# Kernel optimization log

Measured on AMD Instinct MI355X. Metric: run time of the kernel, lower is better.

Reference implementation:

```python
import jax, jax.numpy as jnp
import numpy as np

N_NODES = 50000
N_EDGES = 800000


def setup_inputs() -> dict:
    key = jax.random.key(0)
    ks = jax.random.split(key, 8)
    x = jax.random.normal(ks[0], (N_NODES, 256), dtype=jnp.float32)
    edge_index = jax.random.randint(ks[1], (2, N_EDGES), 0, N_NODES, dtype=jnp.int64)
    edge_weight = jax.random.uniform(ks[2], (N_EDGES,), dtype=jnp.float32)
    # Glorot-style weights for the 3 GCNConv layers: 256->128->64->32
    def glorot(k, fan_in, fan_out):
        s = jnp.sqrt(6.0 / (fan_in + fan_out))
        return jax.random.uniform(k, (fan_in, fan_out), dtype=jnp.float32, minval=-s, maxval=s)
    return {
        "x": x,
        "edge_index": edge_index,
        "edge_weight": edge_weight,
        "W1": glorot(ks[3], 256, 128), "b1": jnp.zeros((128,), jnp.float32),
        "W2": glorot(ks[4], 128, 64),  "b2": jnp.zeros((64,), jnp.float32),
        "W3": glorot(ks[5], 64, 32),   "b3": jnp.zeros((32,), jnp.float32),
    }


def _gcn_forward(x, row, col, ew, params):
    """Stacked GCNConv+ReLU (PyG semantics: add self loops, symmetric norm)."""
    n = x.shape[0]
    loop = jnp.arange(n, dtype=row.dtype)
    row_f = jnp.concatenate([row, loop])            # [E+N] sources
    col_f = jnp.concatenate([col, loop])            # [E+N] targets
    ew_f = jnp.concatenate([ew, jnp.ones((n,), ew.dtype)])
    deg = jax.ops.segment_sum(ew_f, col_f, num_segments=n)
    dinv = jnp.where(deg > 0, jax.lax.rsqrt(deg), 0.0)
    norm = dinv[row_f] * ew_f * dinv[col_f]         # [E+N]
    for W, b in params:
        h = x @ W                                   # [N, d_out] linear first (PyG order)
        msg = h[row_f] * norm[:, None]              # [E+N, d_out] gather + scale
        agg = jax.ops.segment_sum(msg, col_f, num_segments=n)  # scatter-add
        x = jax.nn.relu(agg + b)                    # fused bias + ReLU
    return x


def reference(x, edge_index, edge_weight, W1, b1, W2, b2, W3, b3):
    row, col = edge_index[0], edge_index[1]
    params = [(W1, b1), (W2, b2), (W3, b3)]
    return _gcn_forward(x, row, col, edge_weight, params)
```

## Files before the change

### kernel.cpp

```cpp
#include <hip/hip_runtime.h>
#include <hip/hip_fp16.h>


#define D0 256
#define D1 128
#define D2 64
#define D3 32

#define FIX_SCALE 16777216.0f
#define FIX_INV   (1.0f / 16777216.0f)

typedef _Float16 half8 __attribute__((ext_vector_type(8)));
typedef float floatx4 __attribute__((ext_vector_type(4)));

template <typename SRC>
__device__ __forceinline__ half8 loadA(const SRC* __restrict__ p) {
    if constexpr (sizeof(SRC) == 4) {
        float4 f0 = *(const float4*)p;
        float4 f1 = *(const float4*)(p + 4);
        half8 v;
        v[0] = (_Float16)f0.x; v[1] = (_Float16)f0.y;
        v[2] = (_Float16)f0.z; v[3] = (_Float16)f0.w;
        v[4] = (_Float16)f1.x; v[5] = (_Float16)f1.y;
        v[6] = (_Float16)f1.z; v[7] = (_Float16)f1.w;
        return v;
    } else {
        return *(const half8*)p;
    }
}

template <int K, int BN, typename SRC>
__device__ __forceinline__ void gemm_work(const SRC* __restrict__ X,
                                          const float* __restrict__ W,
                                          _Float16* __restrict__ H, int N,
                                          int w, int totalWaves) {
    constexpr int NC = K / 32;
    constexpr int CG = BN / 32;
    const int lane = threadIdx.x & 63;
    const int quad = lane >> 4;
    const int m = lane & 15;
    const int cg = w & (CG - 1);
    const int nslab = N >> 4;
    const int stride = totalWaves / CG;
    int slab = w / CG;
    if (slab >= nslab) return;
    const int n0 = cg * 32;

    half8 b0[NC], b1[NC];
#pragma unroll
    for (int c = 0; c < NC; ++c) {
#pragma unroll
        for (int j = 0; j < 8; ++j) {
            int k = c * 32 + quad * 8 + j;
            b0[c][j] = (_Float16)W[(size_t)k * BN + n0 + m];
            b1[c][j] = (_Float16)W[(size_t)k * BN + n0 + 16 + m];
        }
    }

    half8 a[NC];
#pragma unroll
    for (int c = 0; c < NC; ++c)
        a[c] = loadA(&X[(size_t)(slab * 16 + m) * K + c * 32 + quad * 8]);

    while (true) {
        const int next = slab + stride;
        half8 an[NC];
        if (next < nslab) {
#pragma unroll
            for (int c = 0; c < NC; ++c)
                an[c] = loadA(&X[(size_t)(next * 16 + m) * K + c * 32 + quad * 8]);
        }

        floatx4 acc0 = (floatx4){0.f, 0.f, 0.f, 0.f};
        floatx4 acc1 = (floatx4){0.f, 0.f, 0.f, 0.f};
#pragma unroll
        for (int c = 0; c < NC; ++c) {
            acc0 = __builtin_amdgcn_mfma_f32_16x16x32_f16(a[c], b0[c], acc0, 0, 0, 0);
            acc1 = __builtin_amdgcn_mfma_f32_16x16x32_f16(a[c], b1[c], acc1, 0, 0, 0);
        }

        const int r0 = slab * 16 + quad * 4;
#pragma unroll
        for (int r = 0; r < 4; ++r) {
            H[(size_t)(r0 + r) * BN + n0 + m]      = (_Float16)acc0[r];
            H[(size_t)(r0 + r) * BN + n0 + 16 + m] = (_Float16)acc1[r];
        }

        if (next >= nslab) break;
        slab = next;
#pragma unroll
        for (int c = 0; c < NC; ++c) a[c] = an[c];
    }
}

__global__ __launch_bounds__(256) void hist_gemm1_kernel(
        const float* __restrict__ x, const float* __restrict__ W1,
        _Float16* __restrict__ h1, int N,
        const int* __restrict__ ei, const float* __restrict__ ew,
        unsigned long long* __restrict__ pk, int* __restrict__ rank, int E,
        int gB) {
    const int b = blockIdx.x;
    if (b < gB) {
        gemm_work<D0, D1, float>(x, W1, h1, N, b * 4 + (threadIdx.x >> 6), gB * 4);
    } else {
        int e = (b - gB) * 256 + threadIdx.x;
        if (e < E) {
            int c = ei[E + e];
            unsigned int wfix = (unsigned int)(ew[e] * FIX_SCALE + 0.5f);
            unsigned long long old =
                atomicAdd(&pk[c], (1ULL << 32) | (unsigned long long)wfix);
            rank[e] = (int)(old >> 32);
        }
    }
}

__global__ __launch_bounds__(256) void scan_reduce(const unsigned long long* __restrict__ pk,
                                                   float* __restrict__ dinv,
                                                   int* __restrict__ cnt,
                                                   int* __restrict__ blockSum, int N) {
    __shared__ int s[256];
    const int t = threadIdx.x;
    const int i = blockIdx.x * 256 + t;
    int v = 0;
    if (i < N) {
        unsigned long long p = pk[i];
        float d = (float)(unsigned int)(p & 0xffffffffULL) * FIX_INV + 1.0f;
        dinv[i] = rsqrtf(d);
        v = (int)(p >> 32);
        cnt[i] = v;
    }
    s[t] = v;
    __syncthreads();
#pragma unroll
    for (int off = 128; off > 0; off >>= 1) {
        if (t < off) s[t] += s[t + off];
        __syncthreads();
    }
    if (t == 0) blockSum[blockIdx.x] = s[0];
}

__global__ __launch_bounds__(256) void scan_apply(const int* __restrict__ cnt,
                                                  const int* __restrict__ blockSum,
                                                  int* __restrict__ row_ptr, int N, int B) {
    __shared__ int bs[256];
    __shared__ int s[256];
    const int t = threadIdx.x;
    bs[t] = (t < B) ? blockSum[t] : 0;
    __syncthreads();
#pragma unroll
    for (int off = 1; off < 256; off <<= 1) {
        int u = (t >= off) ? bs[t - off] : 0;
        __syncthreads();
        bs[t] += u;
        __syncthreads();
    }
    const int myOff = (blockIdx.x > 0) ? bs[blockIdx.x - 1] : 0;
    const int i = blockIdx.x * 256 + t;
    const int v = (i < N) ? cnt[i] : 0;
    s[t] = v;
    __syncthreads();
#pragma unroll
    for (int off = 1; off < 256; off <<= 1) {
        int u = (t >= off) ? s[t - off] : 0;
        __syncthreads();
        s[t] += u;
        __syncthreads();
    }
    if (i < N) row_ptr[i] = s[t] - v + myOff;
    if (blockIdx.x == 0 && t == 0) row_ptr[N] = bs[B - 1];
}

__global__ void fill_kernel(const int* __restrict__ ei, const float* __restrict__ ew,
                            const float* __restrict__ dinv,
                            const int* __restrict__ row_ptr, const int* __restrict__ rank,
                            int2* __restrict__ pairs, int E) {
    int e = blockIdx.x * blockDim.x + threadIdx.x;
    if (e < E) {
        int r = ei[e];
        int c = ei[E + e];
        float w = dinv[r] * ew[e] * dinv[c];
        pairs[row_ptr[c] + rank[e]] = make_int2(r, __float_as_int(w));
    }
}

template <int DIN, int DOUT>
__global__ __launch_bounds__(256) void agg_gemm_kernel(
        const _Float16* __restrict__ H, const int* __restrict__ row_ptr,
        const int2* __restrict__ pairs, const float* __restrict__ dinv,
        const float* __restrict__ bias, const float* __restrict__ W,
        _Float16* __restrict__ Hout, int N) {
    constexpr int TPN = DIN / 8;
    constexpr int NPB = 256 / TPN;
    constexpr int NC  = DIN / 32;
    constexpr int S   = NPB / 16;
    constexpr int T   = DOUT / 16;
    static_assert(S * T == 4, "one tile per wave");
    __shared__ _Float16 sA[NPB][DIN + 8];

    const int tid = threadIdx.x;
    const int g = tid / TPN;
    const int sl = tid % TPN;
    const int node0 = blockIdx.x * NPB;
    const int node = node0 + g;
    const bool valid = node < N;

    const int w = tid >> 6;
    const int lane = tid & 63;
    const int q = lane >> 4;
    const int m = lane & 15;
    const int s = w & (S - 1);
    const int t = w / S;
    half8 bf[NC];
#pragma unroll
    for (int c = 0; c < NC; ++c) {
#pragma unroll
        for (int j = 0; j < 8; ++j)
            bf[c][j] = (_Float16)W[(size_t)(c * 32 + q * 8 + j) * DOUT + t * 16 + m];
    }

    float acc[8];
#pragma unroll
    for (int j = 0; j < 8; ++j) acc[j] = 0.0f;

    int beg = 0, end = 0;
    float di = 0.f;
    half8 uself = (half8){0,0,0,0,0,0,0,0};
    float bb[8];
    if (valid) {
        beg = row_ptr[node];
        end = row_ptr[node + 1];
        di = dinv[node];
        uself = *(const half8*)&H[(size_t)node * DIN + sl * 8];
        *(float4*)&bb[0] = *(const float4*)&bias[sl * 8];
        *(float4*)&bb[4] = *(const float4*)&bias[sl * 8 + 4];
    }

    if (end > beg) {
        const int last = end - 1;
        int2 p0 = pairs[beg];
        int2 p1 = pairs[min(beg + 1, last)];
        int2 p2 = pairs[min(beg + 2, last)];
        int2 p3 = pairs[min(beg + 3, last)];
        int2 p4 = pairs[min(beg + 4, last)];
        half8 u0 = *(const half8*)&H[(size_t)p0.x * DIN + sl * 8];
        half8 u1 = *(const half8*)&H[(size_t)p1.x * DIN + sl * 8];
        half8 u2 = *(const half8*)&H[(size_t)p2.x * DIN + sl * 8];
        half8 u3 = *(const half8*)&H[(size_t)p3.x * DIN + sl * 8];
        for (int k = beg; k < end; ++k) {
            int2 p5 = pairs[min(k + 5, last)];
            half8 u4 = *(const half8*)&H[(size_t)p4.x * DIN + sl * 8];
            float wv = __int_as_float(p0.y);
#pragma unroll
            for (int j = 0; j < 8; ++j) acc[j] = fmaf(wv, (float)u0[j], acc[j]);
            p0 = p1; p1 = p2; p2 = p3; p3 = p4; p4 = p5;
            u0 = u1; u1 = u2; u2 = u3; u3 = u4;
        }
    }

    if (valid) {
        float d2 = di * di;
#pragma unroll
        for (int j = 0; j < 8; ++j) acc[j] = fmaf(d2, (float)uself[j], acc[j]);
        half8 o;
#pragma unroll
        for (int j = 0; j < 8; ++j) o[j] = (_Float16)fmaxf(acc[j] + bb[j], 0.f);
        *(half8*)&sA[g][sl * 8] = o;
    }
    __syncthreads();

    half8 a[NC];
#pragma unroll
    for (int c = 0; c < NC; ++c)
        a[c] = *(const half8*)&sA[s * 16 + m][c * 32 + q * 8];
    floatx4 o4 = (floatx4){0.f, 0.f, 0.f, 0.f};
#pragma unroll
    for (int c = 0; c < NC; ++c)
        o4 = __builtin_amdgcn_mfma_f32_16x16x32_f16(a[c], bf[c], o4, 0, 0, 0);
#pragma unroll
    for (int r = 0; r < 4; ++r) {
        const int nr = node0 + s * 16 + q * 4 + r;
        if (nr < N) Hout[(size_t)nr * DOUT + t * 16 + m] = (_Float16)o4[r];
    }
}

template <int D, typename OUT>
__global__ __launch_bounds__(256) void agg_kernel(const _Float16* __restrict__ H,
                                                  const int* __restrict__ row_ptr,
                                                  const int2* __restrict__ pairs,
                                                  const float* __restrict__ dinv,
                                                  const float* __restrict__ bias,
                                                  OUT* __restrict__ out, int N) {
    constexpr int TPN = D / 8;
    constexpr int NPB = 256 / TPN;
    const int tid = threadIdx.x;
    const int g = tid / TPN;
    const int lane = tid % TPN;
    const int node = blockIdx.x * NPB + g;
    if (node >= N) return;

    const int beg = row_ptr[node];
    const int end = row_ptr[node + 1];
    const float di = dinv[node];
    const half8 uself = *(const half8*)&H[(size_t)node * D + lane * 8];
    float b[8];
    *(float4*)&b[0] = *(const float4*)&bias[lane * 8];
    *(float4*)&b[4] = *(const float4*)&bias[lane * 8 + 4];

    float acc[8];
#pragma unroll
    for (int j = 0; j < 8; ++j) acc[j] = 0.0f;

    if (end > beg) {
        const int last = end - 1;
        int2 p0 = pairs[beg];
        int2 p1 = pairs[min(beg + 1, last)];
        int2 p2 = pairs[min(beg + 2, last)];
        int2 p3 = pairs[min(beg + 3, last)];
        int2 p4 = pairs[min(beg + 4, last)];
        half8 u0 = *(const half8*)&H[(size_t)p0.x * D + lane * 8];
        half8 u1 = *(const half8*)&H[(size_t)p1.x * D + lane * 8];
        half8 u2 = *(const half8*)&H[(size_t)p2.x * D + lane * 8];
        half8 u3 = *(const half8*)&H[(size_t)p3.x * D + lane * 8];
        for (int k = beg; k < end; ++k) {
            int2 p5 = pairs[min(k + 5, last)];
            half8 u4 = *(const half8*)&H[(size_t)p4.x * D + lane * 8];
            float w = __int_as_float(p0.y);
#pragma unroll
            for (int j = 0; j < 8; ++j) acc[j] = fmaf(w, (float)u0[j], acc[j]);
            p0 = p1; p1 = p2; p2 = p3; p3 = p4; p4 = p5;
            u0 = u1; u1 = u2; u2 = u3; u3 = u4;
        }
    }
    const float d2 = di * di;
#pragma unroll
    for (int j = 0; j < 8; ++j) acc[j] = fmaf(d2, (float)uself[j], acc[j]);
#pragma unroll
    for (int j = 0; j < 8; ++j) acc[j] = fmaxf(acc[j] + b[j], 0.f);

    if constexpr (sizeof(OUT) == 2) {
        half8 o;
#pragma unroll
        for (int j = 0; j < 8; ++j) o[j] = (_Float16)acc[j];
        *(half8*)&out[(size_t)node * D + lane * 8] = o;
    } else {
        float* dst = (float*)&out[(size_t)node * D + lane * 8];
        *(float4*)&dst[0] = make_float4(acc[0], acc[1], acc[2], acc[3]);
        *(float4*)&dst[4] = make_float4(acc[4], acc[5], acc[6], acc[7]);
    }
}

extern "C" void kernel_launch(void* const* d_in, const int* in_sizes, int n_in,
                              void* d_out, int out_size, void* d_ws, size_t ws_size,
                              hipStream_t stream) {
    const float* x   = (const float*)d_in[0];
    const int* ei    = (const int*)d_in[1];
    const float* ew  = (const float*)d_in[2];
    const float* W1  = (const float*)d_in[3];
    const float* b1  = (const float*)d_in[4];
    const float* W2  = (const float*)d_in[5];
    const float* b2  = (const float*)d_in[6];
    const float* W3  = (const float*)d_in[7];
    const float* b3  = (const float*)d_in[8];
    float* out = (float*)d_out;

    const int N = in_sizes[0] / D0;
    const int E = in_sizes[2];
    (void)n_in; (void)out_size; (void)ws_size;

    char* ws = (char*)d_ws;
    size_t off = 0;
    auto carve = [&](size_t bytes) -> void* {
        void* p = (void*)(ws + off);
        off += (bytes + 255) & ~(size_t)255;
        return p;
    };
    unsigned long long* pk = (unsigned long long*)carve((size_t)N * 8);
    float* dinv    = (float*)carve((size_t)N * 4);
    int*   cnt     = (int*)carve((size_t)N * 4);
    int*   row_ptr = (int*)carve((size_t)(N + 1) * 4);
    int*   rank    = (int*)carve((size_t)E * 4);
    int*   bsum    = (int*)carve(256 * 4);
    int2*  pairs   = (int2*)carve((size_t)E * 8);
    _Float16* bufH = (_Float16*)carve((size_t)N * D1 * 2);
    _Float16* bufO = (_Float16*)carve((size_t)N * D1 * 2);

    _Float16* h1 = bufH;
    _Float16* h2 = bufO;
    _Float16* h3 = bufH;

    const int eb = (E + 255) / 256;
    const int scanB = (N + 255) / 256;
    const int gB = 768;

    hipMemsetAsync(pk, 0, (size_t)N * 8, stream);
    hist_gemm1_kernel<<<gB + eb, 256, 0, stream>>>(
        x, W1, h1, N, ei, ew, pk, rank, E, gB);

    scan_reduce<<<scanB, 256, 0, stream>>>(pk, dinv, cnt, bsum, N);
    scan_apply<<<scanB, 256, 0, stream>>>(cnt, bsum, row_ptr, N, scanB);
    fill_kernel<<<eb, 256, 0, stream>>>(ei, ew, dinv, row_ptr, rank, pairs, E);

    agg_gemm_kernel<D1, D2><<<(N + 15) / 16, 256, 0, stream>>>(
        h1, row_ptr, pairs, dinv, b1, W2, h2, N);

    agg_gemm_kernel<D2, D3><<<(N + 31) / 32, 256, 0, stream>>>(
        h2, row_ptr, pairs, dinv, b2, W3, h3, N);

    agg_kernel<D3, float><<<(N + 63) / 64, 256, 0, stream>>>(
        h3, row_ptr, pairs, dinv, b3, out, N);
}
```

Baseline: 263.0 us.

## Move layer-1 GEMM into fill kernel with LDS double-buffered X staging

The first-layer GEMM is moved out of the histogram kernel and co-launched with the CSR fill kernel, so the atomic histogram runs alone and the GEMM overlaps the scatter fill instead. The GEMM is also rewritten so a whole block stages a 16-row slab of X into shared memory as fp16, with double buffering, and its four waves each compute a different 32-column group. This aims to get coalesced X loads and to balance the mixed kernels better, at the cost of block-wide syncs and more LDS use.

Result: faster. 253.9 us (-3.5%).

```diff
diff --git a/kernel.cpp b/kernel.cpp
--- a/kernel.cpp
+++ b/kernel.cpp
@@ -13,104 +13,16 @@
 typedef _Float16 half8 __attribute__((ext_vector_type(8)));
 typedef float floatx4 __attribute__((ext_vector_type(4)));
 
-template <typename SRC>
-__device__ __forceinline__ half8 loadA(const SRC* __restrict__ p) {
-    if constexpr (sizeof(SRC) == 4) {
-        float4 f0 = *(const float4*)p;
-        float4 f1 = *(const float4*)(p + 4);
-        half8 v;
-        v[0] = (_Float16)f0.x; v[1] = (_Float16)f0.y;
-        v[2] = (_Float16)f0.z; v[3] = (_Float16)f0.w;
-        v[4] = (_Float16)f1.x; v[5] = (_Float16)f1.y;
-        v[6] = (_Float16)f1.z; v[7] = (_Float16)f1.w;
-        return v;
-    } else {
-        return *(const half8*)p;
-    }
-}
-
-template <int K, int BN, typename SRC>
-__device__ __forceinline__ void gemm_work(const SRC* __restrict__ X,
-                                          const float* __restrict__ W,
-                                          _Float16* __restrict__ H, int N,
-                                          int w, int totalWaves) {
-    constexpr int NC = K / 32;
-    constexpr int CG = BN / 32;
-    const int lane = threadIdx.x & 63;
-    const int quad = lane >> 4;
-    const int m = lane & 15;
-    const int cg = w & (CG - 1);
-    const int nslab = N >> 4;
-    const int stride = totalWaves / CG;
-    int slab = w / CG;
-    if (slab >= nslab) return;
-    const int n0 = cg * 32;
-
-    half8 b0[NC], b1[NC];
-#pragma unroll
-    for (int c = 0; c < NC; ++c) {
-#pragma unroll
-        for (int j = 0; j < 8; ++j) {
-            int k = c * 32 + quad * 8 + j;
-            b0[c][j] = (_Float16)W[(size_t)k * BN + n0 + m];
-            b1[c][j] = (_Float16)W[(size_t)k * BN + n0 + 16 + m];
-        }
-    }
-
-    half8 a[NC];
-#pragma unroll
-    for (int c = 0; c < NC; ++c)
-        a[c] = loadA(&X[(size_t)(slab * 16 + m) * K + c * 32 + quad * 8]);
-
-    while (true) {
-        const int next = slab + stride;
-        half8 an[NC];
-        if (next < nslab) {
-#pragma unroll
-            for (int c = 0; c < NC; ++c)
-                an[c] = loadA(&X[(size_t)(next * 16 + m) * K + c * 32 + quad * 8]);
-        }
-
-        floatx4 acc0 = (floatx4){0.f, 0.f, 0.f, 0.f};
-        floatx4 acc1 = (floatx4){0.f, 0.f, 0.f, 0.f};
-#pragma unroll
-        for (int c = 0; c < NC; ++c) {
-            acc0 = __builtin_amdgcn_mfma_f32_16x16x32_f16(a[c], b0[c], acc0, 0, 0, 0);
-            acc1 = __builtin_amdgcn_mfma_f32_16x16x32_f16(a[c], b1[c], acc1, 0, 0, 0);
-        }
-
-        const int r0 = slab * 16 + quad * 4;
-#pragma unroll
-        for (int r = 0; r < 4; ++r) {
-            H[(size_t)(r0 + r) * BN + n0 + m]      = (_Float16)acc0[r];
-            H[(size_t)(r0 + r) * BN + n0 + 16 + m] = (_Float16)acc1[r];
-        }
-
-        if (next >= nslab) break;
-        slab = next;
-#pragma unroll
-        for (int c = 0; c < NC; ++c) a[c] = an[c];
-    }
-}
-
-__global__ __launch_bounds__(256) void hist_gemm1_kernel(
-        const float* __restrict__ x, const float* __restrict__ W1,
-        _Float16* __restrict__ h1, int N,
+__global__ __launch_bounds__(256) void hist_kernel(
         const int* __restrict__ ei, const float* __restrict__ ew,
-        unsigned long long* __restrict__ pk, int* __restrict__ rank, int E,
-        int gB) {
-    const int b = blockIdx.x;
-    if (b < gB) {
-        gemm_work<D0, D1, float>(x, W1, h1, N, b * 4 + (threadIdx.x >> 6), gB * 4);
-    } else {
-        int e = (b - gB) * 256 + threadIdx.x;
-        if (e < E) {
-            int c = ei[E + e];
-            unsigned int wfix = (unsigned int)(ew[e] * FIX_SCALE + 0.5f);
-            unsigned long long old =
-                atomicAdd(&pk[c], (1ULL << 32) | (unsigned long long)wfix);
-            rank[e] = (int)(old >> 32);
-        }
+        unsigned long long* __restrict__ pk, int* __restrict__ rank, int E) {
+    int e = blockIdx.x * 256 + threadIdx.x;
+    if (e < E) {
+        int c = ei[E + e];
+        unsigned int wfix = (unsigned int)(ew[e] * FIX_SCALE + 0.5f);
+        unsigned long long old =
+            atomicAdd(&pk[c], (1ULL << 32) | (unsigned long long)wfix);
+        rank[e] = (int)(old >> 32);
     }
 }
 
@@ -170,16 +82,97 @@
     if (blockIdx.x == 0 && t == 0) row_ptr[N] = bs[B - 1];
 }
 
-__global__ void fill_kernel(const int* __restrict__ ei, const float* __restrict__ ew,
-                            const float* __restrict__ dinv,
-                            const int* __restrict__ row_ptr, const int* __restrict__ rank,
-                            int2* __restrict__ pairs, int E) {
-    int e = blockIdx.x * blockDim.x + threadIdx.x;
-    if (e < E) {
-        int r = ei[e];
-        int c = ei[E + e];
-        float w = dinv[r] * ew[e] * dinv[c];
-        pairs[row_ptr[c] + rank[e]] = make_int2(r, __float_as_int(w));
+__device__ __forceinline__ void stage_slab(const float* __restrict__ X, int slab,
+                                           _Float16 (*__restrict__ sA)[D0 + 8], int t) {
+    const int row = t >> 4;
+    const int c0 = (t & 15) * 16;
+    const float* src = X + (size_t)(slab * 16 + row) * D0 + c0;
+    float4 f0 = *(const float4*)(src + 0);
+    float4 f1 = *(const float4*)(src + 4);
+    float4 f2 = *(const float4*)(src + 8);
+    float4 f3 = *(const float4*)(src + 12);
+    half8 h0, h1;
+    h0[0] = (_Float16)f0.x; h0[1] = (_Float16)f0.y;
+    h0[2] = (_Float16)f0.z; h0[3] = (_Float16)f0.w;
+    h0[4] = (_Float16)f1.x; h0[5] = (_Float16)f1.y;
+    h0[6] = (_Float16)f1.z; h0[7] = (_Float16)f1.w;
+    h1[0] = (_Float16)f2.x; h1[1] = (_Float16)f2.y;
+    h1[2] = (_Float16)f2.z; h1[3] = (_Float16)f2.w;
+    h1[4] = (_Float16)f3.x; h1[5] = (_Float16)f3.y;
+    h1[6] = (_Float16)f3.z; h1[7] = (_Float16)f3.w;
+    *(half8*)&sA[row][c0]     = h0;
+    *(half8*)&sA[row][c0 + 8] = h1;
+}
+
+__global__ __launch_bounds__(256) void fillgemm_kernel(
+        const float* __restrict__ x, const float* __restrict__ W1,
+        _Float16* __restrict__ h1, int N,
+        const int* __restrict__ ei, const float* __restrict__ ew,
+        const float* __restrict__ dinv, const int* __restrict__ row_ptr,
+        const int* __restrict__ rank, int2* __restrict__ pairs, int E, int gB) {
+    __shared__ _Float16 sA[2][16][D0 + 8];
+    const int b = blockIdx.x;
+    if (b >= gB) {
+        int e = (b - gB) * 256 + threadIdx.x;
+        if (e < E) {
+            int r = ei[e];
+            int c = ei[E + e];
+            float w = dinv[r] * ew[e] * dinv[c];
+            pairs[row_ptr[c] + rank[e]] = make_int2(r, __float_as_int(w));
+        }
+        return;
+    }
+    constexpr int NC = D0 / 32;
+    const int tid = threadIdx.x;
+    const int w = tid >> 6;
+    const int lane = tid & 63;
+    const int quad = lane >> 4;
+    const int m = lane & 15;
+    const int n0 = w * 32;
+
+    half8 b0[NC], b1[NC];
+#pragma unroll
+    for (int c = 0; c < NC; ++c) {
+#pragma unroll
+        for (int j = 0; j < 8; ++j) {
+            int k = c * 32 + quad * 8 + j;
+            b0[c][j] = (_Float16)W1[(size_t)k * D1 + n0 + m];
+            b1[c][j] = (_Float16)W1[(size_t)k * D1 + n0 + 16 + m];
+        }
+    }
+
+    const int nslab = N >> 4;
+    int slab = b;
+    if (slab >= nslab) return;
+    stage_slab(x, slab, sA[0], tid);
+    __syncthreads();
+    int buf = 0;
+    while (true) {
+        const int next = slab + gB;
+        if (next < nslab) stage_slab(x, next, sA[buf ^ 1], tid);
+
+        half8 a[NC];
+#pragma unroll
+        for (int c = 0; c < NC; ++c)
+            a[c] = *(const half8*)&sA[buf][m][c * 32 + quad * 8];
+        floatx4 acc0 = (floatx4){0.f, 0.f, 0.f, 0.f};
+        floatx4 acc1 = (floatx4){0.f, 0.f, 0.f, 0.f};
+#pragma unroll
+        for (int c = 0; c < NC; ++c) {
+            acc0 = __builtin_amdgcn_mfma_f32_16x16x32_f16(a[c], b0[c], acc0, 0, 0, 0);
+            acc1 = __builtin_amdgcn_mfma_f32_16x16x32_f16(a[c], b1[c], acc1, 0, 0, 0);
+        }
+
+        const int r0 = slab * 16 + quad * 4;
+#pragma unroll
+        for (int r = 0; r < 4; ++r) {
+            h1[(size_t)(r0 + r) * D1 + n0 + m]      = (_Float16)acc0[r];
+            h1[(size_t)(r0 + r) * D1 + n0 + 16 + m] = (_Float16)acc1[r];
+        }
+        __syncthreads();
+        if (next >= nslab) break;
+        slab = next;
+        buf ^= 1;
     }
 }
 
@@ -393,12 +386,13 @@
     const int gB = 768;
 
     hipMemsetAsync(pk, 0, (size_t)N * 8, stream);
-    hist_gemm1_kernel<<<gB + eb, 256, 0, stream>>>(
-        x, W1, h1, N, ei, ew, pk, rank, E, gB);
+    hist_kernel<<<eb, 256, 0, stream>>>(ei, ew, pk, rank, E);
 
     scan_reduce<<<scanB, 256, 0, stream>>>(pk, dinv, cnt, bsum, N);
     scan_apply<<<scanB, 256, 0, stream>>>(cnt, bsum, row_ptr, N, scanB);
-    fill_kernel<<<eb, 256, 0, stream>>>(ei, ew, dinv, row_ptr, rank, pairs, E);
+
+    fillgemm_kernel<<<gB + eb, 256, 0, stream>>>(
+        x, W1, h1, N, ei, ew, dinv, row_ptr, rank, pairs, E, gB);
 
     agg_gemm_kernel<D1, D2><<<(N + 15) / 16, 256, 0, stream>>>(
         h1, row_ptr, pairs, dinv, b1, W2, h2, N);
```
